# Kernel tuning notes

Hardware: AMD Instinct MI355X
Metric: run time of the kernel (lower is better)

## Reference

```python
import jax, jax.numpy as jnp
import numpy as np

B, N, C, K, S = 2, 20000, 64, 16, 4  # batch, points, channels, neighbors, share_planes
CS = C // S
EPS = 1e-5


def _gather(x, idx):
    # x: [B, C, N], idx: [B, N, K] -> [B, C, N, K]
    return jax.vmap(lambda xb, ib: xb[:, ib])(x, idx)


def _bn(x, g, b, m, v):
    # inference-mode BatchNorm2d over channel axis 1; x: [B, C, N, K]
    scale = (g / jnp.sqrt(v + EPS))[None, :, None, None]
    return (x - m[None, :, None, None]) * scale + b[None, :, None, None]


def setup_inputs() -> dict:
    key = jax.random.key(0)
    ks = jax.random.split(key, 32)
    d = {}
    d["coord"] = jax.random.normal(ks[0], (B, N, 3), jnp.float32)
    d["q"] = jax.random.normal(ks[1], (B, C, N), jnp.float32)
    d["k"] = jax.random.normal(ks[2], (B, C, N), jnp.float32)
    d["neighbor_indices"] = jax.random.randint(ks[3], (B, N, K), 0, N, jnp.int32)
    sc = 1.0 / np.sqrt(C)
    d["wq"] = jax.random.normal(ks[4], (C, C), jnp.float32) * sc
    d["bq"] = jnp.zeros((C,), jnp.float32)
    d["wk"] = jax.random.normal(ks[5], (C, C), jnp.float32) * sc
    d["bk"] = jnp.zeros((C,), jnp.float32)
    d["wv"] = jax.random.normal(ks[6], (C, C), jnp.float32) * sc
    d["bv"] = jnp.zeros((C,), jnp.float32)
    # linear_p: Conv2d(3,3,1) -> BN(3) -> ReLU -> Conv2d(3,C,1)
    d["p1_w"] = jax.random.normal(ks[7], (3, 3), jnp.float32) * 0.5
    d["p1_b"] = jnp.zeros((3,), jnp.float32)
    d["p_bn_g"] = jnp.ones((3,), jnp.float32)
    d["p_bn_b"] = jnp.zeros((3,), jnp.float32)
    d["p_bn_m"] = jax.random.normal(ks[8], (3,), jnp.float32) * 0.1
    d["p_bn_v"] = jax.random.uniform(ks[9], (3,), jnp.float32) + 0.5
    d["p2_w"] = jax.random.normal(ks[10], (C, 3), jnp.float32) * 0.5
    d["p2_b"] = jnp.zeros((C,), jnp.float32)
    # linear_w: BN(C) -> ReLU -> Conv2d(C, C//S, 1) -> BN(C//S) -> ReLU -> Conv2d(C//S, C//S, 1)
    d["w_bn1_g"] = jnp.ones((C,), jnp.float32)
    d["w_bn1_b"] = jnp.zeros((C,), jnp.float32)
    d["w_bn1_m"] = jax.random.normal(ks[11], (C,), jnp.float32) * 0.1
    d["w_bn1_v"] = jax.random.uniform(ks[12], (C,), jnp.float32) + 0.5
    d["w1_w"] = jax.random.normal(ks[13], (CS, C), jnp.float32) * sc
    d["w1_b"] = jnp.zeros((CS,), jnp.float32)
    d["w_bn2_g"] = jnp.ones((CS,), jnp.float32)
    d["w_bn2_b"] = jnp.zeros((CS,), jnp.float32)
    d["w_bn2_m"] = jax.random.normal(ks[14], (CS,), jnp.float32) * 0.1
    d["w_bn2_v"] = jax.random.uniform(ks[15], (CS,), jnp.float32) + 0.5
    d["w2_w"] = jax.random.normal(ks[16], (CS, CS), jnp.float32) / np.sqrt(CS)
    d["w2_b"] = jnp.zeros((CS,), jnp.float32)
    return d


def reference(coord, q, k, neighbor_indices, wq, bq, wk, bk, wv, bv,
              p1_w, p1_b, p_bn_g, p_bn_b, p_bn_m, p_bn_v, p2_w, p2_b,
              w_bn1_g, w_bn1_b, w_bn1_m, w_bn1_v, w1_w, w1_b,
              w_bn2_g, w_bn2_b, w_bn2_m, w_bn2_v, w2_w, w2_b):
    # 1x1 Conv1d projections: [B, C, N]
    x_q = jnp.einsum('oc,bcn->bon', wq, q) + bq[None, :, None]
    x_k = jnp.einsum('oc,bcn->bon', wk, k) + bk[None, :, None]
    x_v = jnp.einsum('oc,bcn->bon', wv, q) + bv[None, :, None]
    # KNN gathers -> [B, *, N, K]
    p_r = _gather(jnp.swapaxes(coord, 1, 2), neighbor_indices)  # [B, 3, N, K]
    x_k = _gather(x_k, neighbor_indices)                        # [B, C, N, K]
    x_v = _gather(x_v, neighbor_indices)                        # [B, C, N, K]
    # positional MLP
    p_r = jnp.einsum('oc,bcnk->bonk', p1_w, p_r) + p1_b[None, :, None, None]
    p_r = jax.nn.relu(_bn(p_r, p_bn_g, p_bn_b, p_bn_m, p_bn_v))
    p_r = jnp.einsum('oc,bcnk->bonk', p2_w, p_r) + p2_b[None, :, None, None]  # [B, C, N, K]
    # attention weights MLP
    w = x_k - x_q[:, :, :, None] + p_r                          # [B, C, N, K]
    w = jax.nn.relu(_bn(w, w_bn1_g, w_bn1_b, w_bn1_m, w_bn1_v))
    w = jnp.einsum('oc,bcnk->bonk', w1_w, w) + w1_b[None, :, None, None]      # [B, C/S, N, K]
    w = jax.nn.relu(_bn(w, w_bn2_g, w_bn2_b, w_bn2_m, w_bn2_v))
    w = jnp.einsum('oc,bcnk->bonk', w2_w, w) + w2_b[None, :, None, None]
    w = jax.nn.softmax(w, axis=-1)                              # softmax over K
    # grouped weighted sum
    v = jnp.transpose(x_v + p_r, (0, 2, 3, 1)).reshape(B, N, K, S, CS)  # [B, N, K, S, C/S]
    wp = jnp.transpose(w, (0, 2, 3, 1))                                  # [B, N, K, C/S]
    x = jnp.einsum('bnksg,bnkg->bnsg', v, wp).reshape(B, N, C)
    return jnp.transpose(x, (0, 2, 1))  # [B, C, N]
```

## Files before the change

### kernel.cpp

```cpp
#include <hip/hip_runtime.h>
#include <hip/hip_bf16.h>
#include <math.h>

#define B_ 2
#define N_ 20000
#define C_ 64
#define K_ 16
#define CS_ 16
#define EPS_ 1e-5f

typedef float f32x4_t  __attribute__((ext_vector_type(4)));
typedef short bf16x8_t __attribute__((ext_vector_type(8)));
typedef short bf16x4_t __attribute__((ext_vector_type(4)));

__device__ __forceinline__ unsigned int packbf2(float a, float b)
{
    union { __hip_bfloat162 h; unsigned int u; } cv;
    cv.h = __float22bfloat162_rn(float2{a, b});
    return cv.u;
}
__device__ __forceinline__ float bf_lo(unsigned int w)
{
    return __builtin_bit_cast(float, w << 16);
}
__device__ __forceinline__ float bf_hi(unsigned int w)
{
    return __builtin_bit_cast(float, w & 0xFFFF0000u);
}
__device__ __forceinline__ void wave_fence()
{
    __builtin_amdgcn_wave_barrier();
}

__global__ __launch_bounds__(256) void setup_kernel(
    const float* __restrict__ wq, const float* __restrict__ wk,
    const float* __restrict__ wv,
    const float* __restrict__ bq, const float* __restrict__ bk,
    const float* __restrict__ bv,
    const float* __restrict__ w1_w, const float* __restrict__ w1_b,
    const float* __restrict__ w2_w, const float* __restrict__ w2_b,
    const float* __restrict__ w_bn1_g, const float* __restrict__ w_bn1_b,
    const float* __restrict__ w_bn1_m, const float* __restrict__ w_bn1_v,
    const float* __restrict__ w_bn2_g, const float* __restrict__ w_bn2_b,
    const float* __restrict__ w_bn2_m, const float* __restrict__ w_bn2_v,
    const float* __restrict__ p2_w, const float* __restrict__ p2_b,
    uint4* __restrict__ wtab, uint4* __restrict__ a1tab,
    uint2* __restrict__ a2tab, float* __restrict__ cz,
    float4* __restrict__ ctab, float4* __restrict__ ptab)
{
    const int t   = threadIdx.x;
    const int blk = blockIdx.x;
    {
        int e = blk * 256 + t;
        int m = e >> 9, rem = e & 511;
        int og = rem >> 7, half = (rem >> 6) & 1, l = rem & 63;
        const float* W = (m == 0) ? wq : ((m == 1) ? wk : wv);
        const float* base = W + (size_t)(og * 16 + (l & 15)) * C_ + half * 32 + (l >> 4) * 8;
        uint4 o;
        o.x = packbf2(base[0], base[1]); o.y = packbf2(base[2], base[3]);
        o.z = packbf2(base[4], base[5]); o.w = packbf2(base[6], base[7]);
        wtab[e] = o;
    }
    if (blk == 0 && t < 128) {
        int half = t >> 6, l = t & 63;
        const float* base = w1_w + (size_t)(l & 15) * C_ + half * 32 + (l >> 4) * 8;
        uint4 o;
        o.x = packbf2(base[0], base[1]); o.y = packbf2(base[2], base[3]);
        o.z = packbf2(base[4], base[5]); o.w = packbf2(base[6], base[7]);
        a1tab[t] = o;
    }
    if (blk == 1 && t < 64) {
        const float* base = w2_w + (t & 15) * 16 + (t >> 4) * 4;
        uint2 o;
        o.x = packbf2(base[0], base[1]); o.y = packbf2(base[2], base[3]);
        a2tab[t] = o;
    }
    if (blk == 2 && t < 16) {
        float s = w_bn2_g[t] * rsqrtf(w_bn2_v[t] + EPS_);
        cz[t]      = s;
        cz[16 + t] = (w1_b[t] - w_bn2_m[t]) * s + w_bn2_b[t];
        cz[32 + t] = w2_b[t];
    }
    if (blk == 3 && t < 64) {
        float s   = w_bn1_g[t] * rsqrtf(w_bn1_v[t] + EPS_);
        float b1f = w_bn1_b[t] - w_bn1_m[t] * s;
        ctab[t] = float4{s, s * bq[t] - b1f, bk[t], bv[t]};
    }
    if (blk == 4 && t < 64) {
        ptab[t] = float4{p2_w[t*3+0], p2_w[t*3+1], p2_w[t*3+2], p2_b[t]};
    }
}

__global__ __launch_bounds__(256) void proj_kernel(
    const float* __restrict__ q, const float* __restrict__ kin,
    const float* __restrict__ coord,
    const float* __restrict__ p1_w, const float* __restrict__ p1_b,
    const float* __restrict__ p_bn_g, const float* __restrict__ p_bn_b,
    const float* __restrict__ p_bn_m, const float* __restrict__ p_bn_v,
    const uint4* __restrict__ wtab,
    const float4* __restrict__ ctab, const float4* __restrict__ ptab,
    unsigned int* __restrict__ xq2, unsigned int* __restrict__ kv_t)
{
    constexpr int PS = 26;
    __shared__ unsigned int qp[32 * PS];
    __shared__ unsigned int kp[32 * PS];

    const int t   = threadIdx.x;
    const int og  = __builtin_amdgcn_readfirstlane(t >> 6);
    const int l   = t & 63;
    const int col = l & 15;
    const int qd  = l >> 4;
    const int pt0 = blockIdx.x * 16;
    const int pt  = pt0 + col;
    const int b   = pt0 / N_;
    const int n   = pt - b * N_;
    const size_t cb = (size_t)b * C_ * N_ + n;

#pragma unroll
    for (int r = 0; r < 2; r++) {
        int cp = (og << 3) + (qd << 1) + r;
        int ci = cp * 2;
        float q0 = q[cb + (size_t)ci * N_];
        float q1 = q[cb + (size_t)(ci + 1) * N_];
        float k0 = kin[cb + (size_t)ci * N_];
        float k1 = kin[cb + (size_t)(ci + 1) * N_];
        qp[cp * PS + col] = packbf2(q0, q1);
        kp[cp * PS + col] = packbf2(k0, k1);
    }

    union bf8u { bf16x8_t v; uint4 u4; };
    bf8u awq[2], awk[2], awv[2];
#pragma unroll
    for (int half = 0; half < 2; half++) {
        awq[half].u4 = wtab[0 * 512 + og * 128 + half * 64 + l];
        awk[half].u4 = wtab[1 * 512 + og * 128 + half * 64 + l];
        awv[half].u4 = wtab[2 * 512 + og * 128 + half * 64 + l];
    }

    __syncthreads();

    union bf8b { bf16x8_t v; unsigned int u[4]; };
    bf8b bq_[2], bk_[2];
#pragma unroll
    for (int half = 0; half < 2; half++) {
#pragma unroll
        for (int i2 = 0; i2 < 4; i2++) {
            int cp = half * 16 + qd * 4 + i2;
            bq_[half].u[i2] = qp[cp * PS + col];
            bk_[half].u[i2] = kp[cp * PS + col];
        }
    }

    f32x4_t uq = {0.f, 0.f, 0.f, 0.f};
    f32x4_t uv = {0.f, 0.f, 0.f, 0.f};
    f32x4_t uk = {0.f, 0.f, 0.f, 0.f};
    uq = __builtin_amdgcn_mfma_f32_16x16x32_bf16(awq[0].v, bq_[0].v, uq, 0, 0, 0);
    uq = __builtin_amdgcn_mfma_f32_16x16x32_bf16(awq[1].v, bq_[1].v, uq, 0, 0, 0);
    uv = __builtin_amdgcn_mfma_f32_16x16x32_bf16(awv[0].v, bq_[0].v, uv, 0, 0, 0);
    uv = __builtin_amdgcn_mfma_f32_16x16x32_bf16(awv[1].v, bq_[1].v, uv, 0, 0, 0);
    uk = __builtin_amdgcn_mfma_f32_16x16x32_bf16(awk[0].v, bk_[0].v, uk, 0, 0, 0);
    uk = __builtin_amdgcn_mfma_f32_16x16x32_bf16(awk[1].v, bk_[1].v, uk, 0, 0, 0);

    float pbs[3], pbb[3];
#pragma unroll
    for (int j = 0; j < 3; j++) {
        float s = p_bn_g[j] * rsqrtf(p_bn_v[j] + EPS_);
        pbs[j] = s;
        pbb[j] = (p1_b[j] - p_bn_m[j]) * s + p_bn_b[j];
    }
    float cx = coord[pt * 3 + 0], cy = coord[pt * 3 + 1], cz = coord[pt * 3 + 2];
    float h0 = fmaxf(0.f, (p1_w[0]*cx + p1_w[1]*cy + p1_w[2]*cz) * pbs[0] + pbb[0]);
    float h1 = fmaxf(0.f, (p1_w[3]*cx + p1_w[4]*cy + p1_w[5]*cz) * pbs[1] + pbb[1]);
    float h2 = fmaxf(0.f, (p1_w[6]*cx + p1_w[7]*cy + p1_w[8]*cz) * pbs[2] + pbb[2]);

    const int ch0 = og * 16 + qd * 4;
    float xv2[4];
    uint4 kvo;
#pragma unroll
    for (int rr = 0; rr < 4; rr++) {
        const float4 ct  = ctab[ch0 + rr];
        const float4 pt4 = ptab[ch0 + rr];
        float pos = fmaf(pt4.x, h0, fmaf(pt4.y, h1, fmaf(pt4.z, h2, pt4.w)));
        xv2[rr]   = fmaf(ct.x, uq[rr], ct.y);
        float kk  = ct.x * (uk[rr] + ct.z + pos);
        float vv  = uv[rr] + ct.w + pos;
        (&kvo.x)[rr] = packbf2(kk, vv);
    }
    uint2 xqo;
    xqo.x = packbf2(xv2[0], xv2[1]);
    xqo.y = packbf2(xv2[2], xv2[3]);
    *reinterpret_cast<uint2*>(xq2 + (size_t)pt * 32 + (ch0 >> 1)) = xqo;
    *reinterpret_cast<uint4*>(kv_t + (size_t)pt * C_ + ch0) = kvo;
}

#define WROW 72
#define WPN  (K_ * WROW)
#define SS4  20
#define SPN  (K_ * SS4)

__global__ __launch_bounds__(512, 8) void attn_kernel(
    const int* __restrict__ nbr,
    const unsigned int* __restrict__ xq2, const unsigned int* __restrict__ kv_t,
    const uint4* __restrict__ a1tab, const uint2* __restrict__ a2tab,
    const float* __restrict__ cz,
    float* __restrict__ out)
{
    __shared__ unsigned short wlds_all[8 * WPN];
    __shared__ float          sfb_all[8 * SPN];
    __shared__ float          otile[64 * 9];

    const int w  = __builtin_amdgcn_readfirstlane(threadIdx.x >> 6);
    const int l  = threadIdx.x & 63;
    const int al = l & 15;
    const int qd = l >> 4;
    const int cpair = l & 31;
    const int kh    = l >> 5;
    const int c0    = cpair * 2;

    const int pt0 = blockIdx.x * 8;
    const int b   = pt0 / N_;
    const int bB  = b * N_;
    const int bn  = pt0 + w;

    unsigned short* wlds = wlds_all + w * WPN;
    float*          sfb  = sfb_all + w * SPN;

    const int* nb = nbr + (size_t)bn * K_;
    uint2 kvw[8];
#pragma unroll
    for (int j = 0; j < 8; j++) {
        int ia = nb[j];
        int ib = nb[8 + j];
        int idx = (kh != 0) ? ib : ia;
        kvw[j] = *reinterpret_cast<const uint2*>(kv_t + ((size_t)(bB + idx) * C_ + c0));
    }
    const unsigned int xqu = xq2[(size_t)bn * 32 + cpair];
    const float xq0 = bf_lo(xqu);
    const float xq1 = bf_hi(xqu);

    union bf8u { bf16x8_t v; uint4 u4; };
    union bf4u { bf16x4_t v; uint2 u2; };
    bf8u a1q0, a1q1; bf4u a2q;
    a1q0.u4 = a1tab[l];
    a1q1.u4 = a1tab[64 + l];
    a2q.u2  = a2tab[l];
    const float4 zsc4 = *reinterpret_cast<const float4*>(cz + qd * 4);
    const float4 zbi4 = *reinterpret_cast<const float4*>(cz + 16 + qd * 4);
    const float4 tbi4 = *reinterpret_cast<const float4*>(cz + 32 + qd * 4);

#pragma unroll
    for (int j = 0; j < 8; j++) {
        float w0 = fmaxf(0.f, bf_lo(kvw[j].x) - xq0);
        float w1 = fmaxf(0.f, bf_lo(kvw[j].y) - xq1);
        *reinterpret_cast<unsigned int*>(wlds + (kh * 8 + j) * WROW + c0) = packbf2(w0, w1);
    }
    wave_fence();

    const bf16x8_t b0 = *reinterpret_cast<const bf16x8_t*>(wlds + al * WROW + qd * 8);
    const bf16x8_t b1 = *reinterpret_cast<const bf16x8_t*>(wlds + al * WROW + 32 + qd * 8);
    f32x4_t u = {0.f, 0.f, 0.f, 0.f};
    u = __builtin_amdgcn_mfma_f32_16x16x32_bf16(a1q0.v, b0, u, 0, 0, 0);
    u = __builtin_amdgcn_mfma_f32_16x16x32_bf16(a1q1.v, b1, u, 0, 0, 0);

    union { bf16x4_t v; unsigned int u2[2]; } zb;
    {
        float z0 = fmaxf(0.f, u[0] * zsc4.x + zbi4.x);
        float z1 = fmaxf(0.f, u[1] * zsc4.y + zbi4.y);
        float z2 = fmaxf(0.f, u[2] * zsc4.z + zbi4.z);
        float z3 = fmaxf(0.f, u[3] * zsc4.w + zbi4.w);
        zb.u2[0] = packbf2(z0, z1);
        zb.u2[1] = packbf2(z2, z3);
    }

    f32x4_t t4 = {0.f, 0.f, 0.f, 0.f};
    t4 = __builtin_amdgcn_mfma_f32_16x16x16bf16_1k(a2q.v, zb.v, t4, 0, 0, 0);

    float4 sv;
#pragma unroll
    for (int rr = 0; rr < 4; rr++) {
        float e = __expf(t4[rr] + (&tbi4.x)[rr]);
        float s = e;
        s += __shfl_xor(s, 1);
        s += __shfl_xor(s, 2);
        s += __shfl_xor(s, 4);
        s += __shfl_xor(s, 8);
        (&sv.x)[rr] = e * __builtin_amdgcn_rcpf(s);
    }
    *reinterpret_cast<float4*>(sfb + al * SS4 + qd * 4) = sv;
    wave_fence();

    const int g0 = c0 & 15;
    float acc0 = 0.f, acc1 = 0.f;
#pragma unroll
    for (int j = 0; j < 8; j++) {
        float2 sp = *reinterpret_cast<const float2*>(sfb + (kh * 8 + j) * SS4 + g0);
        acc0 = fmaf(bf_hi(kvw[j].x), sp.x, acc0);
        acc1 = fmaf(bf_hi(kvw[j].y), sp.y, acc1);
    }
    acc0 += __shfl_xor(acc0, 32);
    acc1 += __shfl_xor(acc1, 32);
    if (kh == 0) {
        otile[c0 * 9 + w]       = acc0;
        otile[(c0 + 1) * 9 + w] = acc1;
    }
    __syncthreads();

    {
        int c  = threadIdx.x >> 3;
        int nn = threadIdx.x & 7;
        out[(size_t)b * C_ * N_ + (size_t)c * N_ + (pt0 - bB) + nn] = otile[c * 9 + nn];
    }
}

extern "C" void kernel_launch(void* const* d_in, const int* in_sizes, int n_in,
                              void* d_out, int out_size, void* d_ws, size_t ws_size,
                              hipStream_t stream)
{
    const float* coord = (const float*)d_in[0];
    const float* q     = (const float*)d_in[1];
    const float* k     = (const float*)d_in[2];
    const int*   nbr   = (const int*)d_in[3];
    const float* wq = (const float*)d_in[4];
    const float* bq = (const float*)d_in[5];
    const float* wk = (const float*)d_in[6];
    const float* bk = (const float*)d_in[7];
    const float* wv = (const float*)d_in[8];
    const float* bv = (const float*)d_in[9];
    const float* p1_w = (const float*)d_in[10];
    const float* p1_b = (const float*)d_in[11];
    const float* p_bn_g = (const float*)d_in[12];
    const float* p_bn_b = (const float*)d_in[13];
    const float* p_bn_m = (const float*)d_in[14];
    const float* p_bn_v = (const float*)d_in[15];
    const float* p2_w = (const float*)d_in[16];
    const float* p2_b = (const float*)d_in[17];
    const float* w_bn1_g = (const float*)d_in[18];
    const float* w_bn1_b = (const float*)d_in[19];
    const float* w_bn1_m = (const float*)d_in[20];
    const float* w_bn1_v = (const float*)d_in[21];
    const float* w1_w = (const float*)d_in[22];
    const float* w1_b = (const float*)d_in[23];
    const float* w_bn2_g = (const float*)d_in[24];
    const float* w_bn2_b = (const float*)d_in[25];
    const float* w_bn2_m = (const float*)d_in[26];
    const float* w_bn2_v = (const float*)d_in[27];
    const float* w2_w = (const float*)d_in[28];
    const float* w2_b = (const float*)d_in[29];

    const size_t PTS = (size_t)B_ * N_;
    char* wsb = (char*)d_ws;
    unsigned int* kv_t = (unsigned int*)wsb;
    unsigned int* xq2  = (unsigned int*)(wsb + PTS * C_ * 4);
    uint4* wtab  = (uint4*)(wsb + PTS * C_ * 4 + PTS * C_ * 2);
    uint4* a1tab = wtab + 1536;
    uint2* a2tab = (uint2*)(a1tab + 128);
    float* cz    = (float*)(a2tab + 64);
    float4* ctab = (float4*)(cz + 48);
    float4* ptab = ctab + 64;

    setup_kernel<<<6, 256, 0, stream>>>(
        wq, wk, wv, bq, bk, bv, w1_w, w1_b, w2_w, w2_b,
        w_bn1_g, w_bn1_b, w_bn1_m, w_bn1_v,
        w_bn2_g, w_bn2_b, w_bn2_m, w_bn2_v,
        p2_w, p2_b,
        wtab, a1tab, a2tab, cz, ctab, ptab);

    proj_kernel<<<(B_ * N_) / 16, 256, 0, stream>>>(
        q, k, coord,
        p1_w, p1_b, p_bn_g, p_bn_b, p_bn_m, p_bn_v,
        wtab, ctab, ptab, xq2, kv_t);

    attn_kernel<<<(B_ * N_) / 8, 512, 0, stream>>>(
        nbr, xq2, kv_t, a1tab, a2tab, cz,
        (float*)d_out);
}
```

Baseline: 47.12 us.

## Gather four channels per lane with 16-byte loads and use DPP row reductions

```diff
diff --git a/kernel.cpp b/kernel.cpp
--- a/kernel.cpp
+++ b/kernel.cpp
@@ -30,6 +30,20 @@
 __device__ __forceinline__ void wave_fence()
 {
     __builtin_amdgcn_wave_barrier();
+}
+
+__device__ __forceinline__ float row_sum16(float x)
+{
+    float s = x;
+    s += __builtin_bit_cast(float, __builtin_amdgcn_update_dpp(
+            0, __builtin_bit_cast(int, s), 0x128, 0xF, 0xF, false));
+    s += __builtin_bit_cast(float, __builtin_amdgcn_update_dpp(
+            0, __builtin_bit_cast(int, s), 0x124, 0xF, 0xF, false));
+    s += __builtin_bit_cast(float, __builtin_amdgcn_update_dpp(
+            0, __builtin_bit_cast(int, s), 0x122, 0xF, 0xF, false));
+    s += __builtin_bit_cast(float, __builtin_amdgcn_update_dpp(
+            0, __builtin_bit_cast(int, s), 0x121, 0xF, 0xF, false));
+    return s;
 }
 
 __global__ __launch_bounds__(256) void setup_kernel(
@@ -197,6 +211,7 @@
 #define WPN  (K_ * WROW)
 #define SS4  20
 #define SPN  (K_ * SS4)
+#define OS   68
 
 __global__ __launch_bounds__(512, 8) void attn_kernel(
     const int* __restrict__ nbr,
@@ -207,15 +222,17 @@
 {
     __shared__ unsigned short wlds_all[8 * WPN];
     __shared__ float          sfb_all[8 * SPN];
-    __shared__ float          otile[64 * 9];
-
-    const int w  = __builtin_amdgcn_readfirstlane(threadIdx.x >> 6);
-    const int l  = threadIdx.x & 63;
+    __shared__ float          otile[8 * OS];
+
+    const int t  = threadIdx.x;
+    const int w  = __builtin_amdgcn_readfirstlane(t >> 6);
+    const int l  = t & 63;
     const int al = l & 15;
     const int qd = l >> 4;
-    const int cpair = l & 31;
-    const int kh    = l >> 5;
-    const int c0    = cpair * 2;
+    const int cquad = al;
+    const int kq    = qd;
+    const int c0    = cquad * 4;
+    const int g0    = c0 & 15;
 
     const int pt0 = blockIdx.x * 8;
     const int b   = pt0 / N_;
@@ -226,17 +243,15 @@
     float*          sfb  = sfb_all + w * SPN;
 
     const int* nb = nbr + (size_t)bn * K_;
-    uint2 kvw[8];
-#pragma unroll
-    for (int j = 0; j < 8; j++) {
-        int ia = nb[j];
-        int ib = nb[8 + j];
-        int idx = (kh != 0) ? ib : ia;
-        kvw[j] = *reinterpret_cast<const uint2*>(kv_t + ((size_t)(bB + idx) * C_ + c0));
-    }
-    const unsigned int xqu = xq2[(size_t)bn * 32 + cpair];
-    const float xq0 = bf_lo(xqu);
-    const float xq1 = bf_hi(xqu);
+    uint4 kvw[4];
+#pragma unroll
+    for (int j = 0; j < 4; j++) {
+        int idx = nb[kq * 4 + j];
+        kvw[j] = *reinterpret_cast<const uint4*>(kv_t + ((size_t)(bB + idx) * C_ + c0));
+    }
+    const uint2 xqu = *reinterpret_cast<const uint2*>(xq2 + (size_t)bn * 32 + (c0 >> 1));
+    const float xqa = bf_lo(xqu.x), xqb = bf_hi(xqu.x);
+    const float xqc = bf_lo(xqu.y), xqd = bf_hi(xqu.y);
 
     union bf8u { bf16x8_t v; uint4 u4; };
     union bf4u { bf16x4_t v; uint2 u2; };
@@ -249,10 +264,15 @@
     const float4 tbi4 = *reinterpret_cast<const float4*>(cz + 32 + qd * 4);
 
 #pragma unroll
-    for (int j = 0; j < 8; j++) {
-        float w0 = fmaxf(0.f, bf_lo(kvw[j].x) - xq0);
-        float w1 = fmaxf(0.f, bf_lo(kvw[j].y) - xq1);
-        *reinterpret_cast<unsigned int*>(wlds + (kh * 8 + j) * WROW + c0) = packbf2(w0, w1);
+    for (int j = 0; j < 4; j++) {
+        float w0 = fmaxf(0.f, bf_lo(kvw[j].x) - xqa);
+        float w1 = fmaxf(0.f, bf_lo(kvw[j].y) - xqb);
+        float w2 = fmaxf(0.f, bf_lo(kvw[j].z) - xqc);
+        float w3 = fmaxf(0.f, bf_lo(kvw[j].w) - xqd);
+        uint2 wpk;
+        wpk.x = packbf2(w0, w1);
+        wpk.y = packbf2(w2, w3);
+        *reinterpret_cast<uint2*>(wlds + (kq * 4 + j) * WROW + c0) = wpk;
     }
     wave_fence();
 
@@ -279,36 +299,36 @@
 #pragma unroll
     for (int rr = 0; rr < 4; rr++) {
         float e = __expf(t4[rr] + (&tbi4.x)[rr]);
-        float s = e;
-        s += __shfl_xor(s, 1);
-        s += __shfl_xor(s, 2);
-        s += __shfl_xor(s, 4);
-        s += __shfl_xor(s, 8);
+        float s = row_sum16(e);
         (&sv.x)[rr] = e * __builtin_amdgcn_rcpf(s);
     }
     *reinterpret_cast<float4*>(sfb + al * SS4 + qd * 4) = sv;
     wave_fence();
 
-    const int g0 = c0 & 15;
-    float acc0 = 0.f, acc1 = 0.f;
-#pragma unroll
-    for (int j = 0; j < 8; j++) {
-        float2 sp = *reinterpret_cast<const float2*>(sfb + (kh * 8 + j) * SS4 + g0);
-        acc0 = fmaf(bf_hi(kvw[j].x), sp.x, acc0);
-        acc1 = fmaf(bf_hi(kvw[j].y), sp.y, acc1);
-    }
-    acc0 += __shfl_xor(acc0, 32);
-    acc1 += __shfl_xor(acc1, 32);
-    if (kh == 0) {
-        otile[c0 * 9 + w]       = acc0;
-        otile[(c0 + 1) * 9 + w] = acc1;
+    float acc[4] = {0.f, 0.f, 0.f, 0.f};
+#pragma unroll
+    for (int j = 0; j < 4; j++) {
+        const float4 sp = *reinterpret_cast<const float4*>(sfb + (kq * 4 + j) * SS4 + g0);
+        acc[0] = fmaf(bf_hi(kvw[j].x), sp.x, acc[0]);
+        acc[1] = fmaf(bf_hi(kvw[j].y), sp.y, acc[1]);
+        acc[2] = fmaf(bf_hi(kvw[j].z), sp.z, acc[2]);
+        acc[3] = fmaf(bf_hi(kvw[j].w), sp.w, acc[3]);
+    }
+#pragma unroll
+    for (int i = 0; i < 4; i++) {
+        acc[i] += __shfl_xor(acc[i], 16);
+        acc[i] += __shfl_xor(acc[i], 32);
+    }
+    if (kq == 0) {
+        float4 o4 = float4{acc[0], acc[1], acc[2], acc[3]};
+        *reinterpret_cast<float4*>(otile + w * OS + c0) = o4;
     }
     __syncthreads();
 
     {
-        int c  = threadIdx.x >> 3;
-        int nn = threadIdx.x & 7;
-        out[(size_t)b * C_ * N_ + (size_t)c * N_ + (pt0 - bB) + nn] = otile[c * 9 + nn];
+        int c  = t >> 3;
+        int nn = t & 7;
+        out[(size_t)b * C_ * N_ + (size_t)c * N_ + (pt0 - bB) + nn] = otile[nn * OS + c];
     }
 }
 
```

After: 44.66 us, median of 2. -5.2%, faster.
